# Kernel optimization log

Measured on AMD Instinct MI355X. Metric: run time of the kernel, lower is better.

## Reference

```python
import jax, jax.numpy as jnp
import numpy as np

NBIT = 8
NSPLIT = 255.0  # 2**NBIT - 1


def _quantized_matmul(x, w_clean, eps):
    # Faithful port of quantization(): bit-slice x into NBIT binary planes, run a
    # noisy linear per plane with weight w + randn*|w|*0.1, and sum. The 8
    # sequential fc() calls are fused into one einsum over the bit axis.
    # x: (..., in); w_clean: (out, in); eps: (NBIT, out, in) standard normal.
    mn = jnp.min(x)
    mx = jnp.max(x)
    q = ((x - mn) / (mx - mn) * NSPLIT).astype(jnp.uint8).astype(jnp.int32)  # truncating cast as in torch
    quant_base = 2 ** jnp.arange(NBIT, dtype=jnp.int32)
    binary = ((q[..., None] & quant_base) != 0).astype(x.dtype)              # (..., in, NBIT)
    scaled = binary * (2.0 ** jnp.arange(NBIT)).astype(x.dtype)              # plane i scaled by 2**i
    w_noisy = w_clean[None] + eps * jnp.abs(w_clean)[None] * 0.1             # (NBIT, out, in)
    z = jnp.einsum('...ib,boi->...o', scaled, w_noisy)
    return z, mn, mx, w_noisy[-1]  # fc.weight after loop == last noisy weight


def _forward(node_embedding, edge_embedding, nbr_mask, cond1, cond2, eps1, eps2, bn_gamma, bn_beta):
    B, At, Nbr, Fe = edge_embedding.shape
    Fn = node_embedding.shape[-1]
    c1 = jnp.concatenate(
        [jnp.broadcast_to(node_embedding[:, :, None, :], (B, At, Nbr, Fn)), edge_embedding],
        axis=3)                                                              # (B, At, Nbr, Fn+Fe)
    # quantization + re_quantization through fc (re-quant uses last noisy fc.weight)
    z1, mn1, mx1, w_last = _quantized_matmul(c1, cond1[0], eps1)
    bias1 = jnp.sum(mn1 * w_last, axis=1)                                    # (H1,)
    h = jax.nn.relu(z1 / NSPLIT * (mx1 - mn1) + bias1)                       # (B, At, Nbr, H1)
    # quantization + re_quantization through fc_2 (re-quant uses conductance[1][-1])
    z2, mn2, mx2, _ = _quantized_matmul(h, cond2[0], eps2)
    bias2 = jnp.sum(mn2 * cond2[-1], axis=1)                                 # (2*Fn,)
    c2 = z2 / NSPLIT * (mx2 - mn2) + bias2                                   # (B, At, Nbr, 2*Fn)
    nbr_gate, nbr_extract = jnp.split(c2, 2, axis=3)
    nbr_sumed = jax.nn.sigmoid(nbr_gate) * jnp.tanh(nbr_extract) * nbr_mask[..., None]
    nbr_sumed = jnp.sum(nbr_sumed, axis=2)                                   # (B, At, Fn)
    # BatchNorm1d in training mode: batch statistics over flattened (B*At)
    flat = nbr_sumed.reshape(-1, Fn)
    mean = jnp.mean(flat, axis=0)
    var = jnp.var(flat, axis=0)  # biased variance, as torch BN uses for normalization
    bn = ((flat - mean) / jnp.sqrt(var + 1e-5) * bn_gamma + bn_beta).reshape(B, At, Fn)
    return jax.nn.relu(node_embedding + bn)


def setup_inputs() -> dict:
    key = jax.random.key(0)
    ks = jax.random.split(key, 7)
    B, At, Nbr, Fn, Fe = 16, 96, 12, 64, 64
    H1, H2 = 4 * (Fn + Fe), 2 * Fn
    return {
        'node_embedding': jax.random.normal(ks[0], (B, At, Fn), jnp.float32),
        'edge_embedding': jax.random.normal(ks[1], (B, At, Nbr, Fe), jnp.float32),
        'nbr_mask': (jax.random.uniform(ks[2], (B, At, Nbr)) > 0.5).astype(jnp.float32),
        'cond1': jax.random.normal(ks[3], (2, H1, Fn + Fe), jnp.float32) * 0.05,
        'cond2': jax.random.normal(ks[4], (2, H2, H1), jnp.float32) * 0.05,
        'eps1': jax.random.normal(ks[5], (NBIT, H1, Fn + Fe), jnp.float32),
        'eps2': jax.random.normal(ks[6], (NBIT, H2, H1), jnp.float32),
        'bn_gamma': jnp.ones((Fn,), jnp.float32),
        'bn_beta': jnp.zeros((Fn,), jnp.float32),
    }


def reference(node_embedding, edge_embedding, nbr_mask, cond1, cond2, eps1, eps2, bn_gamma, bn_beta):
    return _forward(node_embedding, edge_embedding, nbr_mask, cond1, cond2, eps1, eps2, bn_gamma, bn_beta)
```

## Files before the change

kernel.cpp:

```cpp
#include <hip/hip_runtime.h>
#include <stdint.h>

#define B_    16
#define AT_   96
#define NBR_  12
#define FN_   64
#define FE_   64
#define M1    (B_*AT_*NBR_)
#define R_    (B_*AT_)
#define K1Q   128
#define N1    512
#define K2Q   512
#define N2    128
#define SPLIT2 4

typedef _Float16 f16x8 __attribute__((ext_vector_type(8)));
typedef _Float16 f16x2 __attribute__((ext_vector_type(2)));
typedef float    f32x4 __attribute__((ext_vector_type(4)));

#define OFF_SCAL  0u
#define OFF_B1R   256u
#define OFF_B2R   (OFF_B1R + 2048u)
#define OFF_Q1    4096u
#define OFF_W1E   (OFF_Q1  + (size_t)M1*K1Q)
#define OFF_W2E   (OFF_W1E + (size_t)N1*K1Q*8*2)
#define OFF_Q2    (OFF_W2E + (size_t)N2*K2Q*8*2)
#define OFF_H     (OFF_Q2  + (size_t)M1*K2Q)
#define OFF_ZP    OFF_H
#define OFF_NS    (OFF_H   + (size_t)M1*N1*2)

__device__ __forceinline__ unsigned int enc_f(float f) {
    unsigned int u = __float_as_uint(f);
    return (u & 0x80000000u) ? ~u : (u | 0x80000000u);
}
__device__ __forceinline__ float dec_f(unsigned int u) {
    return __uint_as_float((u & 0x80000000u) ? (u & 0x7FFFFFFFu) : ~u);
}

__global__ void k_init(unsigned int* scal, float* b1raw, float* b2raw) {
    int t = threadIdx.x;
    if (t == 0) { scal[0] = 0xFFFFFFFFu; scal[1] = 0u; scal[2] = 0xFFFFFFFFu; scal[3] = 0u; }
    if (t < N1) b1raw[t] = 0.f;
    if (t < N2) b2raw[t] = 0.f;
}

__global__ __launch_bounds__(256) void k_minmax_c1(const float* __restrict__ node,
                                                   const float* __restrict__ edge,
                                                   unsigned int* __restrict__ scal) {
    const int nn4 = (B_*AT_*FN_)/4;
    const int tot4 = nn4 + (M1*FE_)/4;
    float mn = 3.0e38f, mx = -3.0e38f;
    for (int idx = blockIdx.x*blockDim.x + threadIdx.x; idx < tot4; idx += gridDim.x*blockDim.x) {
        float4 x = (idx < nn4) ? ((const float4*)node)[idx] : ((const float4*)edge)[idx - nn4];
        mn = fminf(mn, fminf(fminf(x.x, x.y), fminf(x.z, x.w)));
        mx = fmaxf(mx, fmaxf(fmaxf(x.x, x.y), fmaxf(x.z, x.w)));
    }
    __shared__ float smn[256], smx[256];
    smn[threadIdx.x] = mn; smx[threadIdx.x] = mx; __syncthreads();
    for (int s = 128; s > 0; s >>= 1) {
        if (threadIdx.x < s) {
            smn[threadIdx.x] = fminf(smn[threadIdx.x], smn[threadIdx.x+s]);
            smx[threadIdx.x] = fmaxf(smx[threadIdx.x], smx[threadIdx.x+s]);
        }
        __syncthreads();
    }
    if (threadIdx.x == 0) { atomicMin(&scal[0], enc_f(smn[0])); atomicMax(&scal[1], enc_f(smx[0])); }
}

template<int KQ, int N, int SBASE, bool USE_SECOND>
__global__ __launch_bounds__(256) void k_prep_w16(const float* __restrict__ w_clean,
                                                  const float* __restrict__ eps,
                                                  const unsigned int* __restrict__ scal,
                                                  float* __restrict__ braw,
                                                  _Float16* __restrict__ We) {
    int idx = blockIdx.x*blockDim.x + threadIdx.x;
    if (idx >= N*KQ) return;
    int o = idx / KQ;
    float mn = dec_f(scal[SBASE]), mx = dec_f(scal[SBASE+1]);
    float s = (mx - mn) * (1.0f/255.0f);
    float w = w_clean[idx];
    float aw = fabsf(w) * 0.1f;
    union { _Float16 h[8]; uint4 u; } pk;
    float p = s;
    float v7 = 0.f;
    #pragma unroll
    for (int b = 0; b < 8; b++) {
        float e = eps[(size_t)b*N*KQ + idx];
        float v = w + e*aw;
        if (b == 7) v7 = v;
        pk.h[b] = (_Float16)(v * p);
        p *= 2.0f;
    }
    *(uint4*)&We[(size_t)idx*8] = pk.u;
    float bv = USE_SECOND ? w_clean[(size_t)N*KQ + idx] : v7;
    #pragma unroll
    for (int off = 32; off > 0; off >>= 1) bv += __shfl_down(bv, off);
    if ((threadIdx.x & 63) == 0) atomicAdd(&braw[o], bv);
}

__global__ __launch_bounds__(256) void k_quant_c1(const float* __restrict__ node,
                                                  const float* __restrict__ edge,
                                                  const unsigned int* __restrict__ scal,
                                                  unsigned int* __restrict__ q1) {
    int idx = blockIdx.x*256 + threadIdx.x;
    int m = idx >> 5, dw = idx & 31;
    const float mn = dec_f(scal[0]), rng = dec_f(scal[1]) - mn;
    float4 x;
    if (dw < 16) x = *(const float4*)&node[(m/NBR_)*FN_ + dw*4];
    else         x = *(const float4*)&edge[(size_t)m*FE_ + (dw-16)*4];
    unsigned int b0 = (unsigned char)(int)((x.x - mn) / rng * 255.0f);
    unsigned int b1 = (unsigned char)(int)((x.y - mn) / rng * 255.0f);
    unsigned int b2 = (unsigned char)(int)((x.z - mn) / rng * 255.0f);
    unsigned int b3 = (unsigned char)(int)((x.w - mn) / rng * 255.0f);
    q1[idx] = b0 | (b1 << 8) | (b2 << 16) | (b3 << 24);
}

__global__ __launch_bounds__(256) void k_quant_h(const _Float16* __restrict__ h,
                                                 const unsigned int* __restrict__ scal,
                                                 unsigned int* __restrict__ q2) {
    int idx = blockIdx.x*256 + threadIdx.x;
    const float mn = dec_f(scal[2]), rng = dec_f(scal[3]) - mn;
    f16x8 v = *(const f16x8*)(h + (size_t)idx*8);
    unsigned int lo = 0, hi = 0;
    #pragma unroll
    for (int j = 0; j < 4; j++) {
        float x = (float)v[j];
        lo |= ((unsigned int)(unsigned char)(int)((x - mn) / rng * 255.0f)) << (j*8);
    }
    #pragma unroll
    for (int j = 0; j < 4; j++) {
        float x = (float)v[4+j];
        hi |= ((unsigned int)(unsigned char)(int)((x - mn) / rng * 255.0f)) << (j*8);
    }
    uint2 o; o.x = lo; o.y = hi;
    *(uint2*)&q2[idx*2] = o;
}

__device__ __forceinline__ f16x8 expand_byte(unsigned int byte) {
    unsigned int r2 = byte | (byte << 15);
    union { unsigned int u[4]; f16x8 h; } t;
    t.u[0] = ( r2       & 0x00010001u) * 0x3C00u;
    t.u[1] = ((r2 >> 2) & 0x00010001u) * 0x3C00u;
    t.u[2] = ((r2 >> 4) & 0x00010001u) * 0x3C00u;
    t.u[3] = ((r2 >> 6) & 0x00010001u) * 0x3C00u;
    return t.h;
}

#define COMPUTE(qd, bf)  do { \
    _Pragma("unroll") for (int kf = 0; kf < 2; ++kf) { \
      _Pragma("unroll") for (int mf = 0; mf < 4; ++mf) { \
        unsigned int byte_ = ((kf ? qd[mf].y : qd[mf].x) >> sh8) & 0xFFu; \
        f16x8 a_ = expand_byte(byte_); \
        _Pragma("unroll") for (int nf = 0; nf < 4; ++nf) \
          acc[mf][nf] = __builtin_amdgcn_mfma_f32_16x16x32_f16(a_, bf[nf*2+kf], acc[mf][nf], 0, 0, 0); \
      } } } while (0)

#define LOADB(bf, itv) { _Pragma("unroll") for (int jb = 0; jb < 8; ++jb) \
    bf[jb] = *(const f16x8*)(W + boff[jb] + (unsigned)(itv)*64); }

#define LOADQ(qd, itv) { _Pragma("unroll") for (int mf = 0; mf < 4; ++mf) \
    qd[mf] = *(const uint2*)(ards + mf*(16*136) + (itv)*8); }

template<int KQ, int N, int SPLITK, bool EPI1>
__global__ __launch_bounds__(256, 2) void kgh(const unsigned char* __restrict__ q,
                                              const _Float16* __restrict__ W,
                                              const float* __restrict__ braw,
                                              void* __restrict__ outv,
                                              unsigned int* __restrict__ scal) {
    constexpr int KP  = KQ * 8;
    constexpr int KPS = KP / SPLITK;
    constexpr int NIT = KPS / 64;
    constexpr int NOT_ = N / 64;
    constexpr int MT  = M1 / 256;
    constexpr int MPX = MT / 8;
    __shared__ __align__(16) unsigned char ldsA[4*64*136];

    const int tid  = threadIdx.x;
    const int lane = tid & 63;
    const int w    = tid >> 6;
    const int l15  = lane & 15;
    const int lq   = lane >> 4;
    const int sh8  = lq * 8;

    const int lin  = blockIdx.x;
    const int xcd  = lin & 7;
    const int jj   = lin >> 3;
    const int mt   = xcd * MPX + (jj % MPX);
    const int rest = jj / MPX;
    const int ot   = rest % NOT_;
    const int zt   = rest / NOT_;

    const int m0    = mt*256 + w*64;
    const int o0    = ot*64;
    const int kbase = zt * KPS;

    unsigned char* wlds = ldsA + w * (64*136);

    {
        const int rsub = lane >> 3;
        const int c    = lane & 7;
        const unsigned int koff = (unsigned int)(kbase >> 3);
        #pragma unroll
        for (int j = 0; j < 8; ++j) {
            const int row = j*8 + rsub;
            uint4 v = *(const uint4*)(q + (size_t)(m0 + row)*KQ + koff + c*16);
            unsigned char* dst = wlds + row*136 + c*16;
            uint2 lo; lo.x = v.x; lo.y = v.y;
            uint2 hi; hi.x = v.z; hi.y = v.w;
            *(uint2*)dst = lo;
            *(uint2*)(dst + 8) = hi;
        }
    }

    f32x4 acc[4][4] = {};

    unsigned int boff[8];
    #pragma unroll
    for (int nf = 0; nf < 4; ++nf)
        #pragma unroll
        for (int kf = 0; kf < 2; ++kf)
            boff[nf*2+kf] = (unsigned int)(o0 + nf*16 + l15) * KP + kbase + kf*32 + lq*8;

    const unsigned char* ards = wlds + l15*136;

    f16x8 bufA[8], bufB[8], bufC[8], bufD[8];
    uint2 qdA[4], qdB[4];
    LOADB(bufA, 0); LOADB(bufB, 1); LOADB(bufC, 2);
    LOADQ(qdA, 0);

    #pragma unroll 1
    for (int it = 0; it < NIT; it += 4) {
        LOADB(bufD, it+3);
        LOADQ(qdB, it+1);
        COMPUTE(qdA, bufA);
        if (it+4 < NIT) LOADB(bufA, it+4);
        LOADQ(qdA, it+2);
        COMPUTE(qdB, bufB);
        if (it+5 < NIT) LOADB(bufB, it+5);
        LOADQ(qdB, it+3);
        COMPUTE(qdA, bufC);
        if (it+6 < NIT) LOADB(bufC, it+6);
        if (it+4 < NIT) LOADQ(qdA, it+4);
        COMPUTE(qdB, bufD);
    }

    if (EPI1) {
        _Float16* out = (_Float16*)outv;
        const float mn1 = dec_f(scal[0]);
        float bv[4];
        #pragma unroll
        for (int nf = 0; nf < 4; ++nf) bv[nf] = mn1 * braw[o0 + nf*16 + l15];
        float tmn = 3.0e38f, tmx = -3.0e38f;
        #pragma unroll
        for (int mf = 0; mf < 4; ++mf) {
            const int mr = m0 + mf*16 + lq*4;
            #pragma unroll
            for (int nf = 0; nf < 4; ++nf) {
                const int oc = o0 + nf*16 + l15;
                #pragma unroll
                for (int r = 0; r < 4; ++r) {
                    float v = fmaxf(acc[mf][nf][r] + bv[nf], 0.0f);
                    _Float16 v16 = (_Float16)v;
                    float vr = (float)v16;
                    tmn = fminf(tmn, vr); tmx = fmaxf(tmx, vr);
                    out[(size_t)(mr + r)*N + oc] = v16;
                }
            }
        }
        float* red = (float*)ldsA;
        __syncthreads();
        red[tid] = tmn; red[256 + tid] = tmx;
        __syncthreads();
        for (int s = 128; s > 0; s >>= 1) {
            if (tid < s) {
                red[tid]       = fminf(red[tid],       red[tid + s]);
                red[256 + tid] = fmaxf(red[256 + tid], red[256 + tid + s]);
            }
            __syncthreads();
        }
        if (tid == 0) { atomicMin(&scal[2], enc_f(red[0])); atomicMax(&scal[3], enc_f(red[256])); }
    } else {
        _Float16* op = (_Float16*)outv + (size_t)zt * ((size_t)M1 * N);
        #pragma unroll
        for (int mf = 0; mf < 4; ++mf) {
            const int mr = m0 + mf*16 + lq*4;
            #pragma unroll
            for (int nf = 0; nf < 4; ++nf) {
                const int oc = o0 + nf*16 + l15;
                #pragma unroll
                for (int r = 0; r < 4; ++r)
                    op[(size_t)(mr + r)*N + oc] = (_Float16)acc[mf][nf][r];
            }
        }
    }
}

__global__ __launch_bounds__(256) void k_nbr(const _Float16* __restrict__ zp,
                                             const float* __restrict__ b2raw,
                                             const unsigned int* __restrict__ scal,
                                             const float* __restrict__ mask,
                                             float* __restrict__ ns) {
    const size_t SP = (size_t)M1 * N2;
    int tid = threadIdx.x;
    int r = blockIdx.x*8 + (tid >> 5);
    int f2 = (tid & 31) * 2;
    const float mn2 = dec_f(scal[2]);
    float bg0 = mn2 * b2raw[f2],      bg1 = mn2 * b2raw[f2+1];
    float be0 = mn2 * b2raw[64 + f2], be1 = mn2 * b2raw[65 + f2];
    float s0 = 0.f, s1 = 0.f;
    #pragma unroll
    for (int n = 0; n < NBR_; n++) {
        int m = r*NBR_ + n;
        size_t base = (size_t)m * N2;
        float g0 = bg0, g1 = bg1, e0 = be0, e1 = be1;
        #pragma unroll
        for (int z = 0; z < SPLIT2; z++) {
            f16x2 gv = *(const f16x2*)(zp + z*SP + base + f2);
            f16x2 ev = *(const f16x2*)(zp + z*SP + base + 64 + f2);
            g0 += (float)gv[0]; g1 += (float)gv[1];
            e0 += (float)ev[0]; e1 += (float)ev[1];
        }
        float mk = mask[m];
        s0 += (1.0f / (1.0f + expf(-g0))) * tanhf(e0) * mk;
        s1 += (1.0f / (1.0f + expf(-g1))) * tanhf(e1) * mk;
    }
    float2 o; o.x = s0; o.y = s1;
    *(float2*)&ns[r*64 + f2] = o;
}

__global__ __launch_bounds__(256) void k_bn(const float* __restrict__ ns,
                                            const float* __restrict__ node,
                                            const float* __restrict__ gamma,
                                            const float* __restrict__ beta,
                                            float* __restrict__ out) {
    int f = blockIdx.x;
    int tid = threadIdx.x;
    float x[6];
    float s = 0.f, ss = 0.f;
    #pragma unroll
    for (int k = 0; k < 6; k++) {
        int r = tid + k*256;
        x[k] = ns[r*64 + f];
        s += x[k]; ss += x[k]*x[k];
    }
    __shared__ float rs[256], rss[256];
    rs[tid] = s; rss[tid] = ss; __syncthreads();
    for (int st = 128; st > 0; st >>= 1) {
        if (tid < st) { rs[tid] += rs[tid+st]; rss[tid] += rss[tid+st]; }
        __syncthreads();
    }
    float mean = rs[0] / 1536.0f;
    float var  = rss[0] / 1536.0f - mean*mean;
    float denom = sqrtf(var + 1e-5f);
    float g = gamma[f], bt = beta[f];
    #pragma unroll
    for (int k = 0; k < 6; k++) {
        int r = tid + k*256;
        float v = node[r*64 + f] + ((x[k] - mean) / denom * g + bt);
        out[r*64 + f] = fmaxf(v, 0.f);
    }
}

extern "C" void kernel_launch(void* const* d_in, const int* in_sizes, int n_in,
                              void* d_out, int out_size, void* d_ws, size_t ws_size,
                              hipStream_t stream) {
    const float* node  = (const float*)d_in[0];
    const float* edge  = (const float*)d_in[1];
    const float* mask  = (const float*)d_in[2];
    const float* cond1 = (const float*)d_in[3];
    const float* cond2 = (const float*)d_in[4];
    const float* eps1  = (const float*)d_in[5];
    const float* eps2  = (const float*)d_in[6];
    const float* gamma = (const float*)d_in[7];
    const float* beta  = (const float*)d_in[8];
    float* out = (float*)d_out;
    char* ws = (char*)d_ws;

    unsigned int*  scal = (unsigned int*)(ws + OFF_SCAL);
    float* b1raw = (float*)(ws + OFF_B1R);
    float* b2raw = (float*)(ws + OFF_B2R);
    unsigned char* q1 = (unsigned char*)(ws + OFF_Q1);
    _Float16* W1e = (_Float16*)(ws + OFF_W1E);
    _Float16* W2e = (_Float16*)(ws + OFF_W2E);
    unsigned char* q2 = (unsigned char*)(ws + OFF_Q2);
    _Float16* h  = (_Float16*)(ws + OFF_H);
    _Float16* zp = (_Float16*)(ws + OFF_ZP);
    float*    ns = (float*)(ws + OFF_NS);

    k_init<<<1, 1024, 0, stream>>>(scal, b1raw, b2raw);
    k_minmax_c1<<<512, 256, 0, stream>>>(node, edge, scal);
    k_prep_w16<K1Q, N1, 0, false><<<(N1*K1Q + 255)/256, 256, 0, stream>>>(cond1, eps1, scal, b1raw, W1e);
    k_quant_c1<<<(M1*32)/256, 256, 0, stream>>>(node, edge, scal, (unsigned int*)q1);
    kgh<K1Q, N1, 1, true><<<576, 256, 0, stream>>>(q1, W1e, b1raw, h, scal);
    k_prep_w16<K2Q, N2, 2, true><<<(N2*K2Q + 255)/256, 256, 0, stream>>>(cond2, eps2, scal, b2raw, W2e);
    k_quant_h<<<(M1*512/8)/256, 256, 0, stream>>>(h, scal, (unsigned int*)q2);
    kgh<K2Q, N2, SPLIT2, false><<<576, 256, 0, stream>>>(q2, W2e, b2raw, zp, scal);
    k_nbr<<<R_/8, 256, 0, stream>>>(zp, b2raw, scal, mask, ns);
    k_bn<<<64, 256, 0, stream>>>(ns, node, gamma, beta, out);
}
```

Baseline: 230.9 us.

## Halve GEMM M-tile per wave, shallow double-buffer pipeline, plain 3D grid

The bit-plane GEMM kernel now gives each wave 32 rows instead of 64, so the block tile becomes 128x64. Its B-operand prefetch drops from four buffers to two, and launch_bounds asks for 3 blocks per SM instead of 2. The XCD-aware block swizzle is replaced with a straightforward 3D grid, which doubles the block count. The aim is higher occupancy and less register pressure. The cost is half the weight reuse per loaded B fragment, a shallower latency-hiding pipeline, and possible loss of L2 locality from dropping the swizzle.

```diff
diff --git a/kernel.cpp b/kernel.cpp
--- a/kernel.cpp
+++ b/kernel.cpp
@@ -148,7 +148,7 @@
 
 #define COMPUTE(qd, bf)  do { \
     _Pragma("unroll") for (int kf = 0; kf < 2; ++kf) { \
-      _Pragma("unroll") for (int mf = 0; mf < 4; ++mf) { \
+      _Pragma("unroll") for (int mf = 0; mf < 2; ++mf) { \
         unsigned int byte_ = ((kf ? qd[mf].y : qd[mf].x) >> sh8) & 0xFFu; \
         f16x8 a_ = expand_byte(byte_); \
         _Pragma("unroll") for (int nf = 0; nf < 4; ++nf) \
@@ -158,11 +158,11 @@
 #define LOADB(bf, itv) { _Pragma("unroll") for (int jb = 0; jb < 8; ++jb) \
     bf[jb] = *(const f16x8*)(W + boff[jb] + (unsigned)(itv)*64); }
 
-#define LOADQ(qd, itv) { _Pragma("unroll") for (int mf = 0; mf < 4; ++mf) \
+#define LOADQ(qd, itv) { _Pragma("unroll") for (int mf = 0; mf < 2; ++mf) \
     qd[mf] = *(const uint2*)(ards + mf*(16*136) + (itv)*8); }
 
 template<int KQ, int N, int SPLITK, bool EPI1>
-__global__ __launch_bounds__(256, 2) void kgh(const unsigned char* __restrict__ q,
+__global__ __launch_bounds__(256, 3) void kgt(const unsigned char* __restrict__ q,
                                               const _Float16* __restrict__ W,
                                               const float* __restrict__ braw,
                                               void* __restrict__ outv,
@@ -170,10 +170,7 @@
     constexpr int KP  = KQ * 8;
     constexpr int KPS = KP / SPLITK;
     constexpr int NIT = KPS / 64;
-    constexpr int NOT_ = N / 64;
-    constexpr int MT  = M1 / 256;
-    constexpr int MPX = MT / 8;
-    __shared__ __align__(16) unsigned char ldsA[4*64*136];
+    __shared__ __align__(16) unsigned char ldsA[4*32*136];
 
     const int tid  = threadIdx.x;
     const int lane = tid & 63;
@@ -181,27 +178,19 @@
     const int l15  = lane & 15;
     const int lq   = lane >> 4;
     const int sh8  = lq * 8;
-
-    const int lin  = blockIdx.x;
-    const int xcd  = lin & 7;
-    const int jj   = lin >> 3;
-    const int mt   = xcd * MPX + (jj % MPX);
-    const int rest = jj / MPX;
-    const int ot   = rest % NOT_;
-    const int zt   = rest / NOT_;
-
-    const int m0    = mt*256 + w*64;
-    const int o0    = ot*64;
+    const int m0    = blockIdx.x * 128 + w * 32;
+    const int o0    = blockIdx.y * 64;
+    const int zt    = blockIdx.z;
     const int kbase = zt * KPS;
 
-    unsigned char* wlds = ldsA + w * (64*136);
+    unsigned char* wlds = ldsA + w * (32*136);
 
     {
         const int rsub = lane >> 3;
         const int c    = lane & 7;
         const unsigned int koff = (unsigned int)(kbase >> 3);
         #pragma unroll
-        for (int j = 0; j < 8; ++j) {
+        for (int j = 0; j < 4; ++j) {
             const int row = j*8 + rsub;
             uint4 v = *(const uint4*)(q + (size_t)(m0 + row)*KQ + koff + c*16);
             unsigned char* dst = wlds + row*136 + c*16;
@@ -212,7 +201,7 @@
         }
     }
 
-    f32x4 acc[4][4] = {};
+    f32x4 acc[2][4] = {};
 
     unsigned int boff[8];
     #pragma unroll
@@ -223,25 +212,21 @@
 
     const unsigned char* ards = wlds + l15*136;
 
-    f16x8 bufA[8], bufB[8], bufC[8], bufD[8];
-    uint2 qdA[4], qdB[4];
-    LOADB(bufA, 0); LOADB(bufB, 1); LOADB(bufC, 2);
+    f16x8 bufA[8], bufB[8];
+    uint2 qdA[2], qdB[2];
+    LOADB(bufA, 0);
     LOADQ(qdA, 0);
 
     #pragma unroll 1
-    for (int it = 0; it < NIT; it += 4) {
-        LOADB(bufD, it+3);
+    for (int it = 0; it < NIT; it += 2) {
+        LOADB(bufB, it+1);
         LOADQ(qdB, it+1);
         COMPUTE(qdA, bufA);
-        if (it+4 < NIT) LOADB(bufA, it+4);
-        LOADQ(qdA, it+2);
+        if (it+2 < NIT) {
+            LOADB(bufA, it+2);
+            LOADQ(qdA, it+2);
+        }
         COMPUTE(qdB, bufB);
-        if (it+5 < NIT) LOADB(bufB, it+5);
-        LOADQ(qdB, it+3);
-        COMPUTE(qdA, bufC);
-        if (it+6 < NIT) LOADB(bufC, it+6);
-        if (it+4 < NIT) LOADQ(qdA, it+4);
-        COMPUTE(qdB, bufD);
     }
 
     if (EPI1) {
@@ -252,7 +237,7 @@
         for (int nf = 0; nf < 4; ++nf) bv[nf] = mn1 * braw[o0 + nf*16 + l15];
         float tmn = 3.0e38f, tmx = -3.0e38f;
         #pragma unroll
-        for (int mf = 0; mf < 4; ++mf) {
+        for (int mf = 0; mf < 2; ++mf) {
             const int mr = m0 + mf*16 + lq*4;
             #pragma unroll
             for (int nf = 0; nf < 4; ++nf) {
@@ -282,7 +267,7 @@
     } else {
         _Float16* op = (_Float16*)outv + (size_t)zt * ((size_t)M1 * N);
         #pragma unroll
-        for (int mf = 0; mf < 4; ++mf) {
+        for (int mf = 0; mf < 2; ++mf) {
             const int mr = m0 + mf*16 + lq*4;
             #pragma unroll
             for (int nf = 0; nf < 4; ++nf) {
@@ -391,10 +376,10 @@
     k_minmax_c1<<<512, 256, 0, stream>>>(node, edge, scal);
     k_prep_w16<K1Q, N1, 0, false><<<(N1*K1Q + 255)/256, 256, 0, stream>>>(cond1, eps1, scal, b1raw, W1e);
     k_quant_c1<<<(M1*32)/256, 256, 0, stream>>>(node, edge, scal, (unsigned int*)q1);
-    kgh<K1Q, N1, 1, true><<<576, 256, 0, stream>>>(q1, W1e, b1raw, h, scal);
+    kgt<K1Q, N1, 1, true><<<dim3(M1/128, N1/64, 1), 256, 0, stream>>>(q1, W1e, b1raw, h, scal);
     k_prep_w16<K2Q, N2, 2, true><<<(N2*K2Q + 255)/256, 256, 0, stream>>>(cond2, eps2, scal, b2raw, W2e);
     k_quant_h<<<(M1*512/8)/256, 256, 0, stream>>>(h, scal, (unsigned int*)q2);
-    kgh<K2Q, N2, SPLIT2, false><<<576, 256, 0, stream>>>(q2, W2e, b2raw, zp, scal);
+    kgt<K2Q, N2, SPLIT2, false><<<dim3(M1/128, N2/64, SPLIT2), 256, 0, stream>>>(q2, W2e, b2raw, zp, scal);
     k_nbr<<<R_/8, 256, 0, stream>>>(zp, b2raw, scal, mask, ns);
     k_bn<<<64, 256, 0, stream>>>(ns, node, gamma, beta, out);
 }
```

Result: slower. 281.4 us (+21.9%).
